# Optimization experiments

Hardware: AMD Instinct MI355X
Metric: run time of the kernel (lower is better)

Reference implementation:

```python
import jax, jax.numpy as jnp
import numpy as np

MAX_DISP = 20  # matches init_kwargs max_displacement


def setup_inputs() -> dict:
    key = jax.random.key(0)
    k1, k2 = jax.random.split(key)
    feat1 = jax.random.normal(k1, (4, 128, 64, 64), dtype=jnp.float32)
    feat2 = jax.random.normal(k2, (4, 128, 64, 64), dtype=jnp.float32)
    return {"feat1": feat1, "feat2": feat2}


def reference(feat1, feat2):
    pad = MAX_DISP
    D = 2 * pad + 1  # displacement window side (41)
    b, c, h, w = feat1.shape
    feat2_pad = jnp.pad(feat2, ((0, 0), (0, 0), (pad, pad), (pad, pad)))

    def step(carry, ij):
        i = ij // D
        j = ij % D
        sl = jax.lax.dynamic_slice(feat2_pad, (0, 0, i, j), (b, c, h, w))
        # dot over channel dim -> [b, h, w]
        return carry, jnp.sum(feat1 * sl, axis=1)

    # scan over all D*D displacements keeps peak memory at one [b,c,h,w] slice
    _, corr = jax.lax.scan(step, None, jnp.arange(D * D))  # [D*D, b, h, w]
    return jnp.transpose(corr, (1, 0, 2, 3))  # [b, D*D, h, w]
```

## Files before the change

### kernel.cpp

```cpp
#include <hip/hip_runtime.h>
#include <stdint.h>


#define NB 4
#define NC 128
#define NH 64
#define NW 64
#define PAD 20
#define ND 41
#define HW (NH * NW)
#define ROW_U4 1024

typedef __attribute__((ext_vector_type(8))) __bf16 bf16x8;
typedef __attribute__((ext_vector_type(16))) float f32x16;

__device__ __forceinline__ void barrier_lds() {
  asm volatile("s_waitcnt lgkmcnt(0)" ::: "memory");
  __builtin_amdgcn_s_barrier();
  asm volatile("" ::: "memory");
}

__device__ __forceinline__ unsigned int pk2(float a, float b) {
  unsigned short lo = __builtin_bit_cast(unsigned short, (__bf16)a);
  unsigned short hi = __builtin_bit_cast(unsigned short, (__bf16)b);
  return (unsigned int)lo | ((unsigned int)hi << 16);
}

__device__ __forceinline__ float f4elem(const float4 v, int j) {
  return j == 0 ? v.x : j == 1 ? v.y : j == 2 ? v.z : v.w;
}

__global__ __launch_bounds__(256) void conv_kernel(
    const float* __restrict__ f1, const float* __restrict__ f2,
    uint4* __restrict__ ws) {
  const int blk = blockIdx.x;
  const int isF2 = blk >> 8;
  const int by = blk & 255;
  const int b = by >> 6, y = by & 63;
  const float* src = (isF2 ? f2 : f1) + (size_t)b * NC * HW + (size_t)y * NW;
  uint4* dst = ws + (size_t)isF2 * (NB * NH * ROW_U4) + (size_t)by * ROW_U4;
  const int xq = threadIdx.x & 15;
  const int cg = threadIdx.x >> 4;
  const float* p = src + (size_t)cg * 8 * HW + xq * 4;
  float4 v[8];
#pragma unroll
  for (int i = 0; i < 8; ++i) v[i] = *(const float4*)(p + (size_t)i * HW);
#pragma unroll
  for (int j = 0; j < 4; ++j) {
    uint4 u;
    u.x = pk2(f4elem(v[0], j), f4elem(v[1], j));
    u.y = pk2(f4elem(v[2], j), f4elem(v[3], j));
    u.z = pk2(f4elem(v[4], j), f4elem(v[5], j));
    u.w = pk2(f4elem(v[6], j), f4elem(v[7], j));
    dst[cg * 64 + xq * 4 + j] = u;
  }
}

__global__ __launch_bounds__(256, 4) void corr_main(
    const uint4* __restrict__ ws, float* __restrict__ out) {
  __shared__ float cbuf[2][64 * 64];

  const int bid = blockIdx.x;
  const int lid = (bid & 7) * 128 + (bid >> 3);
  const int dq = lid & 3;
  const int y = (lid >> 2) & 63;
  const int b = lid >> 8;

  const int t = threadIdx.x;
  const int lane = t & 63;
  const int wv = t >> 6;
  const int I = wv & 1;
  const int J = wv >> 1;
  const int kh = lane >> 5;

  const int xa = I * 32 + (lane & 31);
  const int xb = J * 32 + (lane & 31);
  const int col = (lane & 31) + 32 * J;
  const int rbase = kh * 4 + I * 32;
  const int xg = t & 63;
  const int g = t >> 6;

  const uint4* f1t = ws;
  const uint4* f2t = ws + NB * NH * ROW_U4;

  const int dBeg = (ND * dq) / 4;
  const int dEnd = (ND * (dq + 1)) / 4;
  int a0 = 20 - y;
  if (a0 < dBeg) a0 = dBeg;
  if (a0 > dEnd) a0 = dEnd;
  int a1 = 84 - y;
  if (a1 < a0) a1 = a0;
  if (a1 > dEnd) a1 = dEnd;

  const size_t outBase = (size_t)b * (ND * ND) * HW + (size_t)y * NW;

  for (int di = dBeg; di < a0; ++di) {
    const size_t dB = outBase + (size_t)di * ND * HW;
    for (int k = g; k < ND; k += 4)
      __builtin_nontemporal_store(0.f, &out[dB + (size_t)k * HW + xg]);
  }
  for (int di = a1; di < dEnd; ++di) {
    const size_t dB = outBase + (size_t)di * ND * HW;
    for (int k = g; k < ND; k += 4)
      __builtin_nontemporal_store(0.f, &out[dB + (size_t)k * HW + xg]);
  }
  const int n = a1 - a0;
  if (n <= 0) return;

  const uint4* f1row = f1t + (size_t)(b * 64 + y) * ROW_U4 + kh * 64 + xb;
  bf16x8 bfrag[8];
#pragma unroll
  for (int ks = 0; ks < 8; ++ks)
    bfrag[ks] = __builtin_bit_cast(bf16x8, f1row[ks * 128]);

  const uint4* f2row = f2t + (size_t)(b * 64) * ROW_U4 + kh * 64 + xa;

  int p = 0;
#pragma unroll 1
  for (int j = 0; j < n; ++j) {
    const int yp = y + (a0 + j) - PAD;
    const uint4* ap = f2row + (size_t)yp * ROW_U4;
    uint4 a[8];
#pragma unroll
    for (int ks = 0; ks < 8; ++ks) a[ks] = ap[ks * 128];

    if (j > 0) {
      const size_t dB = outBase + (size_t)(a0 + j - 1) * ND * HW;
      const float* cb = cbuf[p ^ 1];
      for (int k = g; k < ND; k += 4) {
        const int xs = xg + k - PAD;
        const float vv = (xs >= 0 && xs < NW) ? cb[xs * 64 + xg] : 0.f;
        __builtin_nontemporal_store(vv, &out[dB + (size_t)k * HW + xg]);
      }
    }

    f32x16 acc;
#pragma unroll
    for (int r = 0; r < 16; ++r) acc[r] = 0.f;
#pragma unroll
    for (int ks = 0; ks < 8; ++ks)
      acc = __builtin_amdgcn_mfma_f32_32x32x16_bf16(
          __builtin_bit_cast(bf16x8, a[ks]), bfrag[ks], acc, 0, 0, 0);
#pragma unroll
    for (int r = 0; r < 16; ++r) {
      const int row = rbase + (r & 3) + 8 * (r >> 2);
      cbuf[p][row * 64 + col] = acc[r];
    }
    barrier_lds();
    p ^= 1;
  }

  {
    const size_t dB = outBase + (size_t)(a0 + n - 1) * ND * HW;
    const float* cb = cbuf[p ^ 1];
    for (int k = g; k < ND; k += 4) {
      const int xs = xg + k - PAD;
      const float vv = (xs >= 0 && xs < NW) ? cb[xs * 64 + xg] : 0.f;
      __builtin_nontemporal_store(vv, &out[dB + (size_t)k * HW + xg]);
    }
  }
}

__device__ __forceinline__ void convwrite(const float4 (&v)[8],
                                          uint4* __restrict__ lds, int xq,
                                          int cg) {
#pragma unroll
  for (int j = 0; j < 4; ++j) {
    const int x = xq * 4 + j;
    uint4 u;
    u.x = pk2(f4elem(v[0], j), f4elem(v[1], j));
    u.y = pk2(f4elem(v[2], j), f4elem(v[3], j));
    u.z = pk2(f4elem(v[4], j), f4elem(v[5], j));
    u.w = pk2(f4elem(v[6], j), f4elem(v[7], j));
    lds[x * 16 + (cg ^ (x & 7))] = u;
  }
}

__global__ __launch_bounds__(256, 2) void corr_fallback(
    const float* __restrict__ feat1, const float* __restrict__ feat2,
    float* __restrict__ out) {
  __shared__ uint4 f2s[2][64 * 16];
  __shared__ float cbuf[2][64 * 64];

  const int bid = blockIdx.x;
  const int lid = (bid & 7) * 64 + (bid >> 3);
  const int half = lid & 1;
  const int y = (lid >> 1) & 63;
  const int b = lid >> 7;

  const int t = threadIdx.x;
  const int lane = t & 63;
  const int wv = t >> 6;
  const int I = wv & 1;
  const int J = wv >> 1;
  const int xa = I * 32 + (lane & 31);
  const int xb = J * 32 + (lane & 31);
  const int kh = lane >> 5;
  const int aBase = xa * 16, aSw = xa & 7;
  const int bBase = xb * 16, bSw = xb & 7;
  const int col = (lane & 31) + J * 32;
  const int rbase = kh * 4 + I * 32;
  const int xg = t & 63;
  const int g = t >> 6;
  const int xq = t & 15;
  const int cg = t >> 4;
  const size_t rowoff = (size_t)cg * 8 * HW + xq * 4;
  const float* f1row = feat1 + (size_t)b * NC * HW + (size_t)y * NW + rowoff;
  const float* f2row0 = feat2 + (size_t)b * NC * HW + rowoff;
  const size_t outBase = ((size_t)b * (ND * ND) * NH + y) * NW;

  int dBeg, dEnd;
  if (half == 0) {
    dBeg = (y < PAD) ? (PAD - y) : 0;
    dEnd = PAD + 1;
  } else {
    dBeg = PAD + 1;
    const int e = (NH + PAD) - y;
    dEnd = e < ND ? e : ND;
  }
  const int zBeg = half ? dEnd : 0;
  const int zEnd = half ? ND : dBeg;
  for (int di = zBeg; di < zEnd; ++di) {
    const size_t dB = outBase + (size_t)di * ND * HW;
    for (int k = g; k < ND; k += 4) out[dB + (size_t)k * HW + xg] = 0.f;
  }
  if (dBeg >= dEnd) return;

  float4 v[8];
#pragma unroll
  for (int i = 0; i < 8; ++i) v[i] = *(const float4*)(f1row + (size_t)i * HW);
  uint4* f1tmp = (uint4*)&cbuf[0][0];
  convwrite(v, f1tmp, xq, cg);
  {
    const int yp0 = y + dBeg - PAD;
#pragma unroll
    for (int i = 0; i < 8; ++i)
      v[i] = *(const float4*)(f2row0 + (size_t)yp0 * NW + (size_t)i * HW);
  }
  __syncthreads();
  bf16x8 bfrag[8];
#pragma unroll
  for (int ks = 0; ks < 8; ++ks) {
    const int q = ks * 2 + kh;
    bfrag[ks] = __builtin_bit_cast(bf16x8, f1tmp[bBase + (q ^ bSw)]);
  }
  __syncthreads();

  const int nIter = dEnd - dBeg;
  int p = 0;
#pragma unroll 1
  for (int j = 0; j < nIter; ++j) {
    convwrite(v, f2s[p], xq, cg);
    {
      const int nj = (j + 1 < nIter) ? j + 1 : j;
      const int ypn = y + dBeg + nj - PAD;
#pragma unroll
      for (int i = 0; i < 8; ++i)
        v[i] = *(const float4*)(f2row0 + (size_t)ypn * NW + (size_t)i * HW);
    }
    __syncthreads();

    f32x16 acc;
#pragma unroll
    for (int r = 0; r < 16; ++r) acc[r] = 0.f;
#pragma unroll
    for (int ks = 0; ks < 8; ++ks) {
      const int q = ks * 2 + kh;
      bf16x8 aa = __builtin_bit_cast(bf16x8, f2s[p][aBase + (q ^ bSw)]);
      acc = __builtin_amdgcn_mfma_f32_32x32x16_bf16(aa, bfrag[ks], acc, 0, 0, 0);
    }
#pragma unroll
    for (int r = 0; r < 16; ++r) {
      const int row = rbase + (r & 3) + 8 * (r >> 2);
      cbuf[p][row * 64 + col] = acc[r];
    }
    if (j > 0) {
      const size_t dBase = outBase + (size_t)(dBeg + j - 1) * ND * HW;
      const float* cb = cbuf[p ^ 1];
      for (int k = g; k < ND; k += 4) {
        const int xs = xg + k - PAD;
        const float vv = (xs >= 0 && xs < NW) ? cb[xs * 64 + xg] : 0.f;
        out[dBase + (size_t)k * HW + xg] = vv;
      }
    }
    p ^= 1;
  }
  __syncthreads();
  {
    const size_t dBase = outBase + (size_t)(dEnd - 1) * ND * HW;
    const float* cb = cbuf[p ^ 1];
    for (int k = g; k < ND; k += 4) {
      const int xs = xg + k - PAD;
      const float vv = (xs >= 0 && xs < NW) ? cb[xs * 64 + xg] : 0.f;
      out[dBase + (size_t)k * HW + xg] = vv;
    }
  }
}

extern "C" void kernel_launch(void* const* d_in, const int* in_sizes, int n_in,
                              void* d_out, int out_size, void* d_ws,
                              size_t ws_size, hipStream_t stream) {
  (void)in_sizes; (void)n_in; (void)out_size;
  const float* f1 = (const float*)d_in[0];
  const float* f2 = (const float*)d_in[1];
  float* out = (float*)d_out;
  const size_t need = (size_t)2 * NB * NH * ROW_U4 * sizeof(uint4);
  if (ws_size >= need && d_ws != nullptr) {
    uint4* ws = (uint4*)d_ws;
    conv_kernel<<<dim3(512), dim3(256), 0, stream>>>(f1, f2, ws);
    corr_main<<<dim3(NB * NH * 4), dim3(256), 0, stream>>>(ws, out);
  } else {
    corr_fallback<<<dim3(NB * NH * 2), dim3(256), 0, stream>>>(f1, f2, out);
  }
}
```

Measured before the change: 39.94 us.

## Balance correlation work across blocks and move zero-row stores into conversion kernel

```diff
diff --git a/kernel.cpp b/kernel.cpp
--- a/kernel.cpp
+++ b/kernel.cpp
@@ -10,15 +10,19 @@
 #define ND 41
 #define HW (NH * NW)
 #define ROW_U4 1024
+#define VALID_TOTAL 8816
+#define VALID_PER_B 2204
+#define ZERO_TOTAL 1680
+#define ZERO_PER_B 420
 
 typedef __attribute__((ext_vector_type(8))) __bf16 bf16x8;
 typedef __attribute__((ext_vector_type(16))) float f32x16;
 
-__device__ __forceinline__ void barrier_lds() {
-  asm volatile("s_waitcnt lgkmcnt(0)" ::: "memory");
-  __builtin_amdgcn_s_barrier();
-  asm volatile("" ::: "memory");
-}
+__device__ __forceinline__ int cntv(int y) {
+  return (y < 20) ? (21 + y) : ((y < 44) ? 41 : (84 - y));
+}
+__device__ __forceinline__ int va0(int y) { return (y < 20) ? (20 - y) : 0; }
+__device__ __forceinline__ int va1(int y) { return (y < 44) ? 41 : (84 - y); }
 
 __device__ __forceinline__ unsigned int pk2(float a, float b) {
   unsigned short lo = __builtin_bit_cast(unsigned short, (__bf16)a);
@@ -32,27 +36,52 @@
 
 __global__ __launch_bounds__(256) void conv_kernel(
     const float* __restrict__ f1, const float* __restrict__ f2,
-    uint4* __restrict__ ws) {
+    uint4* __restrict__ ws, float* __restrict__ out) {
   const int blk = blockIdx.x;
-  const int isF2 = blk >> 8;
-  const int by = blk & 255;
-  const int b = by >> 6, y = by & 63;
-  const float* src = (isF2 ? f2 : f1) + (size_t)b * NC * HW + (size_t)y * NW;
-  uint4* dst = ws + (size_t)isF2 * (NB * NH * ROW_U4) + (size_t)by * ROW_U4;
-  const int xq = threadIdx.x & 15;
-  const int cg = threadIdx.x >> 4;
-  const float* p = src + (size_t)cg * 8 * HW + xq * 4;
-  float4 v[8];
-#pragma unroll
-  for (int i = 0; i < 8; ++i) v[i] = *(const float4*)(p + (size_t)i * HW);
-#pragma unroll
-  for (int j = 0; j < 4; ++j) {
-    uint4 u;
-    u.x = pk2(f4elem(v[0], j), f4elem(v[1], j));
-    u.y = pk2(f4elem(v[2], j), f4elem(v[3], j));
-    u.z = pk2(f4elem(v[4], j), f4elem(v[5], j));
-    u.w = pk2(f4elem(v[6], j), f4elem(v[7], j));
-    dst[cg * 64 + xq * 4 + j] = u;
+  if (blk < 512) {
+    const int isF2 = blk >> 8;
+    const int by = blk & 255;
+    const int b = by >> 6, y = by & 63;
+    const float* src = (isF2 ? f2 : f1) + (size_t)b * NC * HW + (size_t)y * NW;
+    uint4* dst = ws + (size_t)isF2 * (NB * NH * ROW_U4) + (size_t)by * ROW_U4;
+    const int xq = threadIdx.x & 15;
+    const int cg = threadIdx.x >> 4;
+    const float* p = src + (size_t)cg * 8 * HW + xq * 4;
+    float4 v[8];
+#pragma unroll
+    for (int i = 0; i < 8; ++i) v[i] = *(const float4*)(p + (size_t)i * HW);
+#pragma unroll
+    for (int j = 0; j < 4; ++j) {
+      uint4 u;
+      u.x = pk2(f4elem(v[0], j), f4elem(v[1], j));
+      u.y = pk2(f4elem(v[2], j), f4elem(v[3], j));
+      u.z = pk2(f4elem(v[4], j), f4elem(v[5], j));
+      u.w = pk2(f4elem(v[6], j), f4elem(v[7], j));
+      dst[cg * 64 + xq * 4 + j] = u;
+    }
+  } else {
+    const int z = blk - 512;
+    const int z0 = z * 3 + (z < 144 ? z : 144);
+    const int nz = 3 + (z < 144 ? 1 : 0);
+    const int xg = threadIdx.x & 63;
+    const int g = threadIdx.x >> 6;
+    for (int i = 0; i < nz; ++i) {
+      const int idx = z0 + i;
+      const int b = idx / ZERO_PER_B;
+      int rz = idx - b * ZERO_PER_B;
+      int y = 0;
+      for (;;) {
+        const int zc = (y < 20) ? (20 - y) : ((y >= 44) ? (y - 43) : 0);
+        if (rz < zc) break;
+        rz -= zc;
+        ++y;
+      }
+      const int di = (y < 20) ? rz : (84 - y + rz);
+      const size_t dB =
+          (size_t)b * (ND * ND) * HW + (size_t)di * ND * HW + (size_t)y * NW;
+      for (int k = g; k < ND; k += 4)
+        __builtin_nontemporal_store(0.f, &out[dB + (size_t)k * HW + xg]);
+    }
   }
 }
 
@@ -61,10 +90,21 @@
   __shared__ float cbuf[2][64 * 64];
 
   const int bid = blockIdx.x;
-  const int lid = (bid & 7) * 128 + (bid >> 3);
-  const int dq = lid & 3;
-  const int y = (lid >> 2) & 63;
-  const int b = lid >> 8;
+  const int h = (bid & 7) * 128 + (bid >> 3);
+
+  const int v0 = h * 8 + (h < 624 ? h : 624);
+  const int nTask = 8 + (h < 624 ? 1 : 0);
+
+  int b = v0 / VALID_PER_B;
+  int r = v0 - b * VALID_PER_B;
+  int y = 0;
+  for (;;) {
+    const int c = cntv(y);
+    if (r < c) break;
+    r -= c;
+    ++y;
+  }
+  int di = va0(y) + r;
 
   const int t = threadIdx.x;
   const int lane = t & 63;
@@ -83,80 +123,72 @@
   const uint4* f1t = ws;
   const uint4* f2t = ws + NB * NH * ROW_U4;
 
-  const int dBeg = (ND * dq) / 4;
-  const int dEnd = (ND * (dq + 1)) / 4;
-  int a0 = 20 - y;
-  if (a0 < dBeg) a0 = dBeg;
-  if (a0 > dEnd) a0 = dEnd;
-  int a1 = 84 - y;
-  if (a1 < a0) a1 = a0;
-  if (a1 > dEnd) a1 = dEnd;
-
-  const size_t outBase = (size_t)b * (ND * ND) * HW + (size_t)y * NW;
-
-  for (int di = dBeg; di < a0; ++di) {
-    const size_t dB = outBase + (size_t)di * ND * HW;
-    for (int k = g; k < ND; k += 4)
-      __builtin_nontemporal_store(0.f, &out[dB + (size_t)k * HW + xg]);
-  }
-  for (int di = a1; di < dEnd; ++di) {
-    const size_t dB = outBase + (size_t)di * ND * HW;
-    for (int k = g; k < ND; k += 4)
-      __builtin_nontemporal_store(0.f, &out[dB + (size_t)k * HW + xg]);
-  }
-  const int n = a1 - a0;
-  if (n <= 0) return;
-
   const uint4* f1row = f1t + (size_t)(b * 64 + y) * ROW_U4 + kh * 64 + xb;
+  const uint4* f2row = f2t + (size_t)(b * 64) * ROW_U4 + kh * 64 + xa;
+  size_t outBase = (size_t)b * (ND * ND) * HW + (size_t)y * NW;
   bf16x8 bfrag[8];
 #pragma unroll
   for (int ks = 0; ks < 8; ++ks)
     bfrag[ks] = __builtin_bit_cast(bf16x8, f1row[ks * 128]);
 
-  const uint4* f2row = f2t + (size_t)(b * 64) * ROW_U4 + kh * 64 + xa;
-
   int p = 0;
+  size_t prevDB = 0;
 #pragma unroll 1
-  for (int j = 0; j < n; ++j) {
-    const int yp = y + (a0 + j) - PAD;
+  for (int j = 0; j < nTask; ++j) {
+    const int yp = y + di - PAD;
     const uint4* ap = f2row + (size_t)yp * ROW_U4;
     uint4 a[8];
 #pragma unroll
     for (int ks = 0; ks < 8; ++ks) a[ks] = ap[ks * 128];
 
     if (j > 0) {
-      const size_t dB = outBase + (size_t)(a0 + j - 1) * ND * HW;
       const float* cb = cbuf[p ^ 1];
       for (int k = g; k < ND; k += 4) {
         const int xs = xg + k - PAD;
         const float vv = (xs >= 0 && xs < NW) ? cb[xs * 64 + xg] : 0.f;
-        __builtin_nontemporal_store(vv, &out[dB + (size_t)k * HW + xg]);
+        __builtin_nontemporal_store(vv, &out[prevDB + (size_t)k * HW + xg]);
       }
     }
 
     f32x16 acc;
 #pragma unroll
-    for (int r = 0; r < 16; ++r) acc[r] = 0.f;
+    for (int q = 0; q < 16; ++q) acc[q] = 0.f;
 #pragma unroll
     for (int ks = 0; ks < 8; ++ks)
       acc = __builtin_amdgcn_mfma_f32_32x32x16_bf16(
           __builtin_bit_cast(bf16x8, a[ks]), bfrag[ks], acc, 0, 0, 0);
 #pragma unroll
-    for (int r = 0; r < 16; ++r) {
-      const int row = rbase + (r & 3) + 8 * (r >> 2);
-      cbuf[p][row * 64 + col] = acc[r];
-    }
-    barrier_lds();
+    for (int q = 0; q < 16; ++q) {
+      const int row = rbase + (q & 3) + 8 * (q >> 2);
+      cbuf[p][row * 64 + col] = acc[q];
+    }
+    __syncthreads();
+
+    prevDB = outBase + (size_t)di * ND * HW;
+    ++di;
+    if (di == va1(y) && j + 1 < nTask) {
+      ++y;
+      if (y == 64) {
+        y = 0;
+        ++b;
+      }
+      di = va0(y);
+      f1row = f1t + (size_t)(b * 64 + y) * ROW_U4 + kh * 64 + xb;
+      f2row = f2t + (size_t)(b * 64) * ROW_U4 + kh * 64 + xa;
+      outBase = (size_t)b * (ND * ND) * HW + (size_t)y * NW;
+#pragma unroll
+      for (int ks = 0; ks < 8; ++ks)
+        bfrag[ks] = __builtin_bit_cast(bf16x8, f1row[ks * 128]);
+    }
     p ^= 1;
   }
 
   {
-    const size_t dB = outBase + (size_t)(a0 + n - 1) * ND * HW;
     const float* cb = cbuf[p ^ 1];
     for (int k = g; k < ND; k += 4) {
       const int xs = xg + k - PAD;
       const float vv = (xs >= 0 && xs < NW) ? cb[xs * 64 + xg] : 0.f;
-      __builtin_nontemporal_store(vv, &out[dB + (size_t)k * HW + xg]);
+      __builtin_nontemporal_store(vv, &out[prevDB + (size_t)k * HW + xg]);
     }
   }
 }
@@ -262,17 +294,17 @@
 
     f32x16 acc;
 #pragma unroll
-    for (int r = 0; r < 16; ++r) acc[r] = 0.f;
+    for (int q = 0; q < 16; ++q) acc[q] = 0.f;
 #pragma unroll
     for (int ks = 0; ks < 8; ++ks) {
       const int q = ks * 2 + kh;
-      bf16x8 aa = __builtin_bit_cast(bf16x8, f2s[p][aBase + (q ^ bSw)]);
+      bf16x8 aa = __builtin_bit_cast(bf16x8, f2s[p][aBase + (q ^ aSw)]);
       acc = __builtin_amdgcn_mfma_f32_32x32x16_bf16(aa, bfrag[ks], acc, 0, 0, 0);
     }
 #pragma unroll
-    for (int r = 0; r < 16; ++r) {
-      const int row = rbase + (r & 3) + 8 * (r >> 2);
-      cbuf[p][row * 64 + col] = acc[r];
+    for (int q = 0; q < 16; ++q) {
+      const int row = rbase + (q & 3) + 8 * (q >> 2);
+      cbuf[p][row * 64 + col] = acc[q];
     }
     if (j > 0) {
       const size_t dBase = outBase + (size_t)(dBeg + j - 1) * ND * HW;
@@ -307,8 +339,8 @@
   const size_t need = (size_t)2 * NB * NH * ROW_U4 * sizeof(uint4);
   if (ws_size >= need && d_ws != nullptr) {
     uint4* ws = (uint4*)d_ws;
-    conv_kernel<<<dim3(512), dim3(256), 0, stream>>>(f1, f2, ws);
-    corr_main<<<dim3(NB * NH * 4), dim3(256), 0, stream>>>(ws, out);
+    conv_kernel<<<dim3(1024), dim3(256), 0, stream>>>(f1, f2, ws, out);
+    corr_main<<<dim3(1024), dim3(256), 0, stream>>>(ws, out);
   } else {
     corr_fallback<<<dim3(NB * NH * 2), dim3(256), 0, stream>>>(f1, f2, out);
   }
```

Result: slower. 45.34 us (+13.5%).
